# Optimization experiments

Measured on AMD Instinct MI355X. Metric: run time of the kernel, lower is better.

The kernel has to match this reference:

```python
import jax, jax.numpy as jnp
import numpy as np
import math

THETA = 10000.0

def apply_rope(x, start_pos=0):
    # x: [B, H, S, D], rotate-half RoPE
    B, H, S, D = x.shape
    pos = jnp.arange(start_pos, start_pos + S, dtype=jnp.float32)
    inv_freq = 1.0 / (THETA ** (jnp.arange(0, D, 2, dtype=jnp.float32) / D))  # [D/2]
    ang = pos[:, None] * inv_freq[None, :]  # [S, D/2]
    cos, sin = jnp.cos(ang), jnp.sin(ang)
    x1, x2 = jnp.split(x, 2, axis=-1)
    return jnp.concatenate([x1 * cos - x2 * sin, x1 * sin + x2 * cos], axis=-1)


def setup_inputs() -> dict:
    key = jax.random.key(0)
    ks = jax.random.split(key, 9)
    B, S, E, H, D = 2, 2048, 2048, 16, 128
    s = 0.02
    return {
        "x": jax.random.normal(ks[0], (B, S, E), jnp.float32),
        "W_q": jax.random.normal(ks[1], (E, H * D), jnp.float32) * s,
        "b_q": jnp.zeros((H * D,), jnp.float32),
        "W_k": jax.random.normal(ks[2], (E, D), jnp.float32) * s,
        "b_k": jnp.zeros((D,), jnp.float32),
        "W_v": jax.random.normal(ks[3], (E, D), jnp.float32) * s,
        "b_v": jnp.zeros((D,), jnp.float32),
        "W_o": jax.random.normal(ks[4], (H * D, E), jnp.float32) * s,
        "b_o": jnp.zeros((E,), jnp.float32),
    }


def reference(x, W_q, b_q, W_k, b_k, W_v, b_v, W_o, b_o):
    B, S, E = x.shape
    D = W_k.shape[1]
    H = W_q.shape[1] // D
    # projections (weights stored [in, out])
    q = (x @ W_q + b_q).reshape(B, S, H, D).transpose(0, 2, 1, 3)   # [B,H,S,D]
    k = (x @ W_k + b_k).reshape(B, S, 1, D).transpose(0, 2, 1, 3)   # [B,1,S,D]
    v = (x @ W_v + b_v).reshape(B, S, 1, D).transpose(0, 2, 1, 3)   # [B,1,S,D]
    # RoPE (cache is None -> start_pos = 0)
    q = apply_rope(q, 0)
    k = apply_rope(k, 0)
    # shared-KV attention: k head dim broadcasts over H q heads
    scores = jnp.einsum("bhqd,bokd->bhqk", q, k) / math.sqrt(D)     # [B,H,S,S]
    causal = jnp.tril(jnp.ones((S, S), dtype=bool))
    scores = jnp.where(causal, scores, -jnp.inf)
    attn = jax.nn.softmax(scores, axis=-1)
    out = jnp.einsum("bhqk,bokd->bhqd", attn, v)                    # [B,H,S,D]
    out = out.transpose(0, 2, 1, 3).reshape(B, S, H * D)
    out = out @ W_o + b_o                                           # dropout is identity in eval
    return out
```

## Files before the change

### kernel.cpp

```cpp
#include <hip/hip_runtime.h>
#include <stdint.h>

typedef __bf16 bf16x8 __attribute__((ext_vector_type(8)));
typedef __bf16 bf16x2 __attribute__((ext_vector_type(2)));
typedef float  f32x4  __attribute__((ext_vector_type(4)));
typedef short  s16x8  __attribute__((ext_vector_type(8)));

__device__ inline unsigned short f2b(float f) {
  unsigned int u = __builtin_bit_cast(unsigned int, f);
  u += 0x7FFFu + ((u >> 16) & 1u);
  return (unsigned short)(u >> 16);
}
__device__ inline float b2f(unsigned short h) {
  unsigned int u = ((unsigned int)h) << 16;
  return __builtin_bit_cast(float, u);
}
__device__ inline unsigned int pkcvt(float a, float b) {
  bf16x2 t;
  t[0] = (__bf16)a;
  t[1] = (__bf16)b;
  return __builtin_bit_cast(unsigned int, t);
}
__device__ inline void gload_lds16(const void* g, void* l) {
  __builtin_amdgcn_global_load_lds(
      (const __attribute__((address_space(1))) unsigned int*)g,
      (__attribute__((address_space(3))) unsigned int*)l, 16, 0, 0);
}

__global__ void k_cvt_bf16(const float* __restrict__ in, unsigned short* __restrict__ out, int n4) {
  int i = blockIdx.x * blockDim.x + threadIdx.x;
  if (i < n4) {
    float4 v = ((const float4*)in)[i];
    ushort4 o;
    o.x = f2b(v.x); o.y = f2b(v.y); o.z = f2b(v.z); o.w = f2b(v.w);
    ((ushort4*)out)[i] = o;
  }
}

__global__ void k_transpose(const float* __restrict__ Wq, const float* __restrict__ Wk,
                            const float* __restrict__ Wv, const float* __restrict__ Wo,
                            unsigned short* __restrict__ dstQKV, unsigned short* __restrict__ dstO) {
  __shared__ float tile[32][33];
  int n0 = blockIdx.x * 32;
  int k0 = blockIdx.y * 32;
  const float* src; int ldn, noff, K;
  unsigned short* dst;
  if (blockIdx.z == 0) {
    K = 2048; dst = dstQKV;
    if (n0 < 2048)       { src = Wq; ldn = 2048; noff = n0; }
    else if (n0 < 2176)  { src = Wk; ldn = 128;  noff = n0 - 2048; }
    else                 { src = Wv; ldn = 128;  noff = n0 - 2176; }
  } else {
    if (n0 >= 2048) return;
    K = 2048; dst = dstO;
    src = Wo; ldn = 2048; noff = n0;
  }
  int tx = threadIdx.x & 31, ty = threadIdx.x >> 5;
  for (int yy = ty; yy < 32; yy += 8)
    tile[yy][tx] = src[(size_t)(k0 + yy) * ldn + noff + tx];
  __syncthreads();
  for (int yy = ty; yy < 32; yy += 8)
    dst[(size_t)(n0 + yy) * K + k0 + tx] = f2b(tile[tx][yy]);
}

__global__ void k_bias_concat(const float* __restrict__ bq, const float* __restrict__ bk,
                              const float* __restrict__ bv, float* __restrict__ dst) {
  int i = blockIdx.x * 256 + threadIdx.x;
  if (i < 2304) dst[i] = (i < 2048) ? bq[i] : (i < 2176 ? bk[i - 2048] : bv[i - 2176]);
}

template<int OUT_BF16>
__global__ __launch_bounds__(256)
void k_gemm_lds(const unsigned short* __restrict__ A, const unsigned short* __restrict__ Bt,
                const float* __restrict__ bias, void* __restrict__ Cout,
                int M, int N, int K) {
  __shared__ unsigned short As[3][4096];
  __shared__ unsigned short Bs[3][4096];
  const int tid  = threadIdx.x;
  const int lane = tid & 63, wid = tid >> 6;
  const int lr = lane & 15, lk = lane >> 4;
  const int wr = wid >> 1,  wc = wid & 1;
  const int mb = blockIdx.y * 128, nb = blockIdx.x * 128;

  const int srow = tid >> 2, scb = (tid & 3) * 8;
  const size_t gA = (size_t)(mb + srow) * K + scb;
  const size_t gB = (size_t)(nb + srow) * K + scb;
  const int ldso = wid * 512;

  f32x4 acc[4][4];
  #pragma unroll
  for (int i = 0; i < 4; ++i)
    #pragma unroll
    for (int j = 0; j < 4; ++j) acc[i][j] = (f32x4){0.f, 0.f, 0.f, 0.f};

  auto stage = [&](int buf, int kt) {
    const size_t ko = (size_t)kt * 32;
    gload_lds16(A  + gA + ko,                  &As[buf][ldso]);
    gload_lds16(A  + gA + 64 * (size_t)K + ko, &As[buf][2048 + ldso]);
    gload_lds16(Bt + gB + ko,                  &Bs[buf][ldso]);
    gload_lds16(Bt + gB + 64 * (size_t)K + ko, &Bs[buf][2048 + ldso]);
  };

  const int ktn = K >> 5;
  stage(0, 0);
  stage(1, 1);

  int cur = 0;
  #pragma unroll 1
  for (int kt = 0; kt < ktn; ++kt) {
    if (kt + 2 < ktn) {
      int nbuf = cur + 2; if (nbuf >= 3) nbuf -= 3;
      stage(nbuf, kt + 2);
      asm volatile("s_waitcnt vmcnt(8)" ::: "memory");
    } else if (kt + 1 < ktn) {
      asm volatile("s_waitcnt vmcnt(4)" ::: "memory");
    } else {
      asm volatile("s_waitcnt vmcnt(0)" ::: "memory");
    }
    __builtin_amdgcn_sched_barrier(0);
    __builtin_amdgcn_s_barrier();
    bf16x8 af[4], bfv[4];
    #pragma unroll
    for (int m = 0; m < 4; ++m)
      af[m]  = *(const bf16x8*)&As[cur][(wr * 64 + m * 16 + lr) * 32 + lk * 8];
    #pragma unroll
    for (int n = 0; n < 4; ++n)
      bfv[n] = *(const bf16x8*)&Bs[cur][(wc * 64 + n * 16 + lr) * 32 + lk * 8];
    #pragma unroll
    for (int m = 0; m < 4; ++m)
      #pragma unroll
      for (int n = 0; n < 4; ++n)
        acc[m][n] = __builtin_amdgcn_mfma_f32_16x16x32_bf16(af[m], bfv[n], acc[m][n], 0, 0, 0);
    __builtin_amdgcn_s_barrier();
    ++cur; if (cur == 3) cur = 0;
  }

  const int r0 = mb + wr * 64, c0 = nb + wc * 64;
  #pragma unroll
  for (int m = 0; m < 4; ++m) {
    #pragma unroll
    for (int n = 0; n < 4; ++n) {
      int col = c0 + n * 16 + lr;
      float bb = bias[col];
      #pragma unroll
      for (int r = 0; r < 4; ++r) {
        int row = r0 + m * 16 + lk * 4 + r;
        float v = acc[m][n][r] + bb;
        if (OUT_BF16) ((unsigned short*)Cout)[(size_t)row * N + col] = f2b(v);
        else          ((float*)Cout)[(size_t)row * N + col] = v;
      }
    }
  }
}

__global__ void k_rope(const unsigned short* __restrict__ qkv,
                       unsigned short* __restrict__ qr,
                       unsigned short* __restrict__ kr,
                       int S, int H) {
  int R = blockIdx.x * 4 + (threadIdx.x >> 6);
  int lane = threadIdx.x & 63;
  int per_b = S * (H + 1);
  int b = R / per_b;
  int rem = R - b * per_b;
  int s = rem / (H + 1);
  int j = rem - s * (H + 1);
  const unsigned short* src = qkv + (size_t)(b * S + s) * 2304 + (j < H ? j * 128 : 2048);
  float x1 = b2f(src[lane]);
  float x2 = b2f(src[lane + 64]);
  float invf = expf(-(float)lane * (9.210340371976184f / 64.0f));
  float ang = (float)s * invf;
  float c = cosf(ang), sn = sinf(ang);
  float o1 = x1 * c - x2 * sn;
  float o2 = x1 * sn + x2 * c;
  unsigned short* dst;
  if (j < H) {
    const float scale = 0.08838834764831845f;
    o1 *= scale; o2 *= scale;
    dst = qr + ((size_t)(b * H + j) * S + s) * 128;
  } else {
    dst = kr + ((size_t)(b * S) + s) * 128;
  }
  dst[lane]      = f2b(o1);
  dst[lane + 64] = f2b(o2);
}

__global__ void k_vtrans(const unsigned short* __restrict__ qkv,
                         unsigned short* __restrict__ vt, int S) {
  __shared__ unsigned short tile[32][33];
  int b = blockIdx.z;
  int s0 = blockIdx.x * 32, d0 = blockIdx.y * 32;
  int tx = threadIdx.x & 31, ty = threadIdx.x >> 5;
  for (int yy = ty; yy < 32; yy += 8)
    tile[yy][tx] = qkv[(size_t)(b * S + s0 + yy) * 2304 + 2176 + d0 + tx];
  __syncthreads();
  for (int yy = ty; yy < 32; yy += 8)
    vt[((size_t)b * 128 + d0 + yy) * S + s0 + tx] = tile[tx][yy];
}

__global__ __launch_bounds__(256, 2)
void k_attn(const unsigned short* __restrict__ qr,
            const unsigned short* __restrict__ kr,
            const unsigned short* __restrict__ vt,
            unsigned short* __restrict__ attn_out,
            int S, int H) {
  const int b = blockIdx.z, h = blockIdx.y;
  const int qt = blockIdx.z ? (int)blockIdx.x : (gridDim.x - 1 - (int)blockIdx.x);
  const int qb0 = qt * 128;
  const int tid = threadIdx.x, wid = tid >> 6, lane = tid & 63;
  const int lr = lane & 15, lk = lane >> 4;
  const int qw = qb0 + wid * 32;

  __shared__ unsigned short Kt[2][64 * 128];
  __shared__ unsigned short Vt[2][128 * 64];

  const char* kbyte = (const char*)(kr + (size_t)b * S * 128);
  const char* vbyte = (const char*)(vt + (size_t)b * 128 * S);
  const size_t vrow_bytes = (size_t)S * 2;

  bf16x8 aq[2][4];
  #pragma unroll
  for (int g = 0; g < 2; ++g) {
    const unsigned short* qptr = qr + ((size_t)(b * H + h) * S + (qw + g * 16 + lr)) * 128;
    #pragma unroll
    for (int kk = 0; kk < 4; ++kk) aq[g][kk] = *(const bf16x8*)(qptr + kk * 32 + lk * 8);
  }

  f32x4 accO[2][8];
  #pragma unroll
  for (int g = 0; g < 2; ++g)
    #pragma unroll
    for (int t = 0; t < 8; ++t) accO[g][t] = (f32x4){0.f, 0.f, 0.f, 0.f};
  float lsum[2] = {0.f, 0.f};

  const int vsw = ((lr & 3) | ((lr >> 1) & 4)) << 4;
  int krow_[4], ksw_[4];
  #pragma unroll
  for (int m = 0; m < 4; ++m) {
    int row = ((m >> 1) << 5) + ((m & 1) << 2) + ((lr >> 2) << 3) + (lr & 3);
    krow_[m] = row;
    ksw_[m] = ((row & 3) | ((row >> 1) & 4)) << 4;
  }

  auto stage = [&](int buf, int kb) {
    const char* kg = kbyte + (size_t)kb * 256;
    #pragma unroll
    for (int r = 0; r < 4; ++r) {
      int row = (tid >> 4) + r * 16;
      int sw = ((row & 3) | ((row >> 1) & 4)) << 4;
      const char* src = kg + row * 256 + (((tid & 15) << 4) ^ sw);
      gload_lds16(src, (void*)((char*)&Kt[buf][0] + r * 4096 + wid * 1024));
    }
    const char* vg = vbyte + (size_t)kb * 2;
    #pragma unroll
    for (int r = 0; r < 4; ++r) {
      int d = (tid >> 3) + r * 32;
      int sw = ((d & 3) | ((d >> 1) & 4)) << 4;
      const char* src = vg + (size_t)d * vrow_bytes + (((tid & 7) << 4) ^ sw);
      gload_lds16(src, (void*)((char*)&Vt[buf][0] + r * 4096 + wid * 1024));
    }
  };

  const int nkv = (qb0 + 128) >> 6;
  stage(0, 0);
  int cur = 0;

  #pragma unroll 1
  for (int it = 0; it < nkv; ++it) {
    const int kb = it << 6;
    if (it + 1 < nkv) {
      stage(cur ^ 1, (it + 1) << 6);
      asm volatile("s_waitcnt vmcnt(8)" ::: "memory");
    } else {
      asm volatile("s_waitcnt vmcnt(0)" ::: "memory");
    }
    __builtin_amdgcn_sched_barrier(0);
    __builtin_amdgcn_s_barrier();

    if (kb <= qw + 31) {
      const unsigned short* Kc = &Kt[cur][0];
      const unsigned short* Vc = &Vt[cur][0];

      f32x4 s4[2][4];
      #pragma unroll
      for (int g = 0; g < 2; ++g)
        #pragma unroll
        for (int m = 0; m < 4; ++m) s4[g][m] = (f32x4){0.f, 0.f, 0.f, 0.f};
      __builtin_amdgcn_s_setprio(1);
      #pragma unroll
      for (int kk = 0; kk < 4; ++kk) {
        bf16x8 kfk[4];
        #pragma unroll
        for (int m = 0; m < 4; ++m)
          kfk[m] = *(const bf16x8*)((const char*)Kc + krow_[m] * 256 + ((kk * 64 + lk * 16) ^ ksw_[m]));
        #pragma unroll
        for (int m = 0; m < 4; ++m) {
          s4[0][m] = __builtin_amdgcn_mfma_f32_16x16x32_bf16(kfk[m], aq[0][kk], s4[0][m], 0, 0, 0);
          s4[1][m] = __builtin_amdgcn_mfma_f32_16x16x32_bf16(kfk[m], aq[1][kk], s4[1][m], 0, 0, 0);
        }
      }
      __builtin_amdgcn_s_setprio(0);

      bf16x8 pa[2][2];
      #pragma unroll
      for (int g = 0; g < 2; ++g) {
        const int rowq = qw + g * 16 + lr;
        const bool domask = (kb + 64) > (qw + g * 16);
        uint2 pk[4];
        #pragma unroll
        for (int m = 0; m < 4; ++m) {
          const int kb_m = kb + ((m >> 1) << 5) + ((m & 1) << 2) + lk * 8;
          float p[4];
          #pragma unroll
          for (int r = 0; r < 4; ++r) {
            float v = __expf(s4[g][m][r]);
            if (domask && (kb_m + r) > rowq) v = 0.f;
            p[r] = v;
            lsum[g] += v;
          }
          pk[m].x = pkcvt(p[0], p[1]);
          pk[m].y = pkcvt(p[2], p[3]);
        }
        uint4 ua, ub;
        ua.x = pk[0].x; ua.y = pk[0].y; ua.z = pk[1].x; ua.w = pk[1].y;
        ub.x = pk[2].x; ub.y = pk[2].y; ub.z = pk[3].x; ub.w = pk[3].y;
        pa[g][0] = __builtin_bit_cast(bf16x8, ua);
        pa[g][1] = __builtin_bit_cast(bf16x8, ub);
      }

      __builtin_amdgcn_s_setprio(1);
      #pragma unroll
      for (int t = 0; t < 8; ++t) {
        const char* vl = (const char*)(Vc + (t * 16 + lr) * 64);
        bf16x8 bv0 = *(const bf16x8*)(vl + ((lk * 16) ^ vsw));
        bf16x8 bv1 = *(const bf16x8*)(vl + ((64 + lk * 16) ^ vsw));
        accO[0][t] = __builtin_amdgcn_mfma_f32_16x16x32_bf16(pa[0][0], bv0, accO[0][t], 0, 0, 0);
        accO[1][t] = __builtin_amdgcn_mfma_f32_16x16x32_bf16(pa[1][0], bv0, accO[1][t], 0, 0, 0);
        accO[0][t] = __builtin_amdgcn_mfma_f32_16x16x32_bf16(pa[0][1], bv1, accO[0][t], 0, 0, 0);
        accO[1][t] = __builtin_amdgcn_mfma_f32_16x16x32_bf16(pa[1][1], bv1, accO[1][t], 0, 0, 0);
      }
      __builtin_amdgcn_s_setprio(0);
    }
    __builtin_amdgcn_s_barrier();
    cur ^= 1;
  }

  #pragma unroll
  for (int g = 0; g < 2; ++g) {
    float ls = lsum[g];
    ls += __shfl_xor(ls, 16);
    ls += __shfl_xor(ls, 32);
    float rl[4];
    #pragma unroll
    for (int r = 0; r < 4; ++r) rl[r] = 1.0f / __shfl(ls, lk * 4 + r);
    #pragma unroll
    for (int t = 0; t < 8; ++t) {
      #pragma unroll
      for (int r = 0; r < 4; ++r) {
        int srow = qw + g * 16 + lk * 4 + r;
        float o = accO[g][t][r] * rl[r];
        attn_out[((size_t)(b * S) + srow) * 2048 + h * 128 + t * 16 + lr] = f2b(o);
      }
    }
  }
}

extern "C" void kernel_launch(void* const* d_in, const int* in_sizes, int n_in,
                              void* d_out, int out_size, void* d_ws, size_t ws_size,
                              hipStream_t stream) {
  const float* x  = (const float*)d_in[0];
  const float* Wq = (const float*)d_in[1];
  const float* bq = (const float*)d_in[2];
  const float* Wk = (const float*)d_in[3];
  const float* bk = (const float*)d_in[4];
  const float* Wv = (const float*)d_in[5];
  const float* bv = (const float*)d_in[6];
  const float* Wo = (const float*)d_in[7];
  const float* bo = (const float*)d_in[8];

  const int B = 2, S = 2048, E = 2048, H = 16, D = 128;
  const int M = B * S;
  const int Nqkv = H * D + 2 * D;

  char* w = (char*)d_ws;
  unsigned short* xb    = (unsigned short*)w;
  unsigned short* WqkvT = (unsigned short*)(w + 16777216);
  unsigned short* qkv   = (unsigned short*)(w + 16777216 + 9437184);
  unsigned short* qr    = (unsigned short*)(w + 16777216 + 9437184 + 18874368);
  unsigned short* kr    = qr + (size_t)B * H * S * D;
  unsigned short* vtb   = kr + (size_t)B * S * D;
  float*          cbias = (float*)(vtb + (size_t)B * S * D);
  unsigned short* WoT   = (unsigned short*)(cbias + 4096);
  unsigned short* attn_out = xb;

  k_cvt_bf16<<<dim3((M * E / 4) / 256), 256, 0, stream>>>(x, xb, M * E / 4);
  k_transpose<<<dim3(Nqkv / 32, E / 32, 2), 256, 0, stream>>>(Wq, Wk, Wv, Wo, WqkvT, WoT);
  k_bias_concat<<<dim3(9), 256, 0, stream>>>(bq, bk, bv, cbias);
  k_gemm_lds<1><<<dim3(Nqkv / 128, M / 128), 256, 0, stream>>>(xb, WqkvT, cbias, (void*)qkv, M, Nqkv, E);
  k_rope<<<dim3(B * S * (H + 1) / 4), 256, 0, stream>>>(qkv, qr, kr, S, H);
  k_vtrans<<<dim3(S / 32, D / 32, B), 256, 0, stream>>>(qkv, vtb, S);
  k_attn<<<dim3(S / 128, H, B), 256, 0, stream>>>(qr, kr, vtb, attn_out, S, H);
  k_gemm_lds<0><<<dim3(E / 128, M / 128), 256, 0, stream>>>(attn_out, WoT, bo, (void*)d_out, M, E, H * D);
}
```

Baseline: 216.3 us.

## Pair causal query tiles per block with split-KV across two wave groups

The attention kernel now processes two query tiles per 512-thread block, a long tile (15-xp) and a short tile (xp), so every block does the same total causal work. Each 4-wave group walks a fixed 17-iteration KV schedule: group 0 handles the first half of tile A's KV range, and group 1 handles the rest of tile A and then all of tile B. The two partial results for tile A are combined through LDS at the end, which relies on the kernel having no running max (plain exp-sum). This is meant to remove the load imbalance from causal masking and the tail effect. In exchange it uses 128KB of LDS per block, doubles accumulator registers, and hardcodes S=2048 (the constants 15 and 17).

```diff
diff --git a/kernel.cpp b/kernel.cpp
--- a/kernel.cpp
+++ b/kernel.cpp
@@ -197,40 +197,56 @@
     vt[((size_t)b * 128 + d0 + yy) * S + s0 + tx] = tile[tx][yy];
 }
 
-__global__ __launch_bounds__(256, 2)
+__global__ __launch_bounds__(512, 2)
 void k_attn(const unsigned short* __restrict__ qr,
             const unsigned short* __restrict__ kr,
             const unsigned short* __restrict__ vt,
             unsigned short* __restrict__ attn_out,
             int S, int H) {
   const int b = blockIdx.z, h = blockIdx.y;
-  const int qt = blockIdx.z ? (int)blockIdx.x : (gridDim.x - 1 - (int)blockIdx.x);
-  const int qb0 = qt * 128;
+  const int xp = blockIdx.x;
+  const int qtA = 15 - xp;
+  const int qb0A = qtA * 128, qb0B = xp * 128;
+  const int nh = 2 * qtA + 2;
   const int tid = threadIdx.x, wid = tid >> 6, lane = tid & 63;
+  const int grp = wid >> 2, w4 = wid & 3;
   const int lr = lane & 15, lk = lane >> 4;
-  const int qw = qb0 + wid * 32;
-
-  __shared__ unsigned short Kt[2][64 * 128];
-  __shared__ unsigned short Vt[2][128 * 64];
+  const int gtid = tid & 255;
+
+  __shared__ __align__(16) char ldsbuf[131072];
+  char* gbase = ldsbuf + grp * 65536;
 
   const char* kbyte = (const char*)(kr + (size_t)b * S * 128);
   const char* vbyte = (const char*)(vt + (size_t)b * 128 * S);
   const size_t vrow_bytes = (size_t)S * 2;
 
-  bf16x8 aq[2][4];
-  #pragma unroll
-  for (int g = 0; g < 2; ++g) {
-    const unsigned short* qptr = qr + ((size_t)(b * H + h) * S + (qw + g * 16 + lr)) * 128;
-    #pragma unroll
-    for (int kk = 0; kk < 4; ++kk) aq[g][kk] = *(const bf16x8*)(qptr + kk * 32 + lk * 8);
-  }
-
-  f32x4 accO[2][8];
+  bf16x8 aqA[2][4], aqB[2][4];
+  {
+    const unsigned short* qa = qr + ((size_t)(b * H + h) * S + qb0A + w4 * 32) * 128;
+    #pragma unroll
+    for (int g = 0; g < 2; ++g)
+      #pragma unroll
+      for (int kk = 0; kk < 4; ++kk)
+        aqA[g][kk] = *(const bf16x8*)(qa + (size_t)(g * 16 + lr) * 128 + kk * 32 + lk * 8);
+    if (grp == 1) {
+      const unsigned short* qb = qr + ((size_t)(b * H + h) * S + qb0B + w4 * 32) * 128;
+      #pragma unroll
+      for (int g = 0; g < 2; ++g)
+        #pragma unroll
+        for (int kk = 0; kk < 4; ++kk)
+          aqB[g][kk] = *(const bf16x8*)(qb + (size_t)(g * 16 + lr) * 128 + kk * 32 + lk * 8);
+    }
+  }
+
+  f32x4 accA[2][8], accB[2][8];
   #pragma unroll
   for (int g = 0; g < 2; ++g)
     #pragma unroll
-    for (int t = 0; t < 8; ++t) accO[g][t] = (f32x4){0.f, 0.f, 0.f, 0.f};
-  float lsum[2] = {0.f, 0.f};
+    for (int t = 0; t < 8; ++t) {
+      accA[g][t] = (f32x4){0.f, 0.f, 0.f, 0.f};
+      accB[g][t] = (f32x4){0.f, 0.f, 0.f, 0.f};
+    }
+  float lsA[2] = {0.f, 0.f}, lsB[2] = {0.f, 0.f};
 
   const int vsw = ((lr & 3) | ((lr >> 1) & 4)) << 4;
   int krow_[4], ksw_[4];
@@ -245,120 +261,174 @@
     const char* kg = kbyte + (size_t)kb * 256;
     #pragma unroll
     for (int r = 0; r < 4; ++r) {
-      int row = (tid >> 4) + r * 16;
+      int row = (gtid >> 4) + r * 16;
       int sw = ((row & 3) | ((row >> 1) & 4)) << 4;
-      const char* src = kg + row * 256 + (((tid & 15) << 4) ^ sw);
-      gload_lds16(src, (void*)((char*)&Kt[buf][0] + r * 4096 + wid * 1024));
+      const char* src = kg + row * 256 + (((gtid & 15) << 4) ^ sw);
+      gload_lds16(src, (void*)(gbase + buf * 16384 + r * 4096 + w4 * 1024));
     }
     const char* vg = vbyte + (size_t)kb * 2;
     #pragma unroll
     for (int r = 0; r < 4; ++r) {
-      int d = (tid >> 3) + r * 32;
+      int d = (gtid >> 3) + r * 32;
       int sw = ((d & 3) | ((d >> 1) & 4)) << 4;
-      const char* src = vg + (size_t)d * vrow_bytes + (((tid & 7) << 4) ^ sw);
-      gload_lds16(src, (void*)((char*)&Vt[buf][0] + r * 4096 + wid * 1024));
+      const char* src = vg + (size_t)d * vrow_bytes + (((gtid & 7) << 4) ^ sw);
+      gload_lds16(src, (void*)(gbase + 32768 + buf * 16384 + r * 4096 + w4 * 1024));
     }
   };
 
-  const int nkv = (qb0 + 128) >> 6;
-  stage(0, 0);
+  auto itemKb = [&](int j, int& which) -> int {
+    if (grp == 0) { which = 0; return j * 64; }
+    int idx = 17 + j;
+    if (idx < nh) { which = 0; return idx * 64; }
+    which = 1; return (idx - nh) * 64;
+  };
+
+  auto computeTile = [&](const unsigned short* Kc, const unsigned short* Vc,
+                         int kb, int qb0cur, bf16x8 (&aq)[2][4],
+                         f32x4 (&acc)[2][8], float (&ls)[2]) {
+    const int qw = qb0cur + w4 * 32;
+    if (kb > qw + 31) return;
+    f32x4 s4[2][4];
+    #pragma unroll
+    for (int g = 0; g < 2; ++g)
+      #pragma unroll
+      for (int m = 0; m < 4; ++m) s4[g][m] = (f32x4){0.f, 0.f, 0.f, 0.f};
+    __builtin_amdgcn_s_setprio(1);
+    #pragma unroll
+    for (int kk = 0; kk < 4; ++kk) {
+      bf16x8 kfk[4];
+      #pragma unroll
+      for (int m = 0; m < 4; ++m)
+        kfk[m] = *(const bf16x8*)((const char*)Kc + krow_[m] * 256 + ((kk * 64 + lk * 16) ^ ksw_[m]));
+      #pragma unroll
+      for (int m = 0; m < 4; ++m) {
+        s4[0][m] = __builtin_amdgcn_mfma_f32_16x16x32_bf16(kfk[m], aq[0][kk], s4[0][m], 0, 0, 0);
+        s4[1][m] = __builtin_amdgcn_mfma_f32_16x16x32_bf16(kfk[m], aq[1][kk], s4[1][m], 0, 0, 0);
+      }
+    }
+    __builtin_amdgcn_s_setprio(0);
+    bf16x8 pa[2][2];
+    #pragma unroll
+    for (int g = 0; g < 2; ++g) {
+      const int rowq = qw + g * 16 + lr;
+      const bool domask = (kb + 64) > (qw + g * 16);
+      uint2 pk[4];
+      #pragma unroll
+      for (int m = 0; m < 4; ++m) {
+        const int kb_m = kb + ((m >> 1) << 5) + ((m & 1) << 2) + lk * 8;
+        float p[4];
+        #pragma unroll
+        for (int r = 0; r < 4; ++r) {
+          float v = __expf(s4[g][m][r]);
+          if (domask && (kb_m + r) > rowq) v = 0.f;
+          p[r] = v;
+          ls[g] += v;
+        }
+        pk[m].x = pkcvt(p[0], p[1]);
+        pk[m].y = pkcvt(p[2], p[3]);
+      }
+      uint4 ua, ub;
+      ua.x = pk[0].x; ua.y = pk[0].y; ua.z = pk[1].x; ua.w = pk[1].y;
+      ub.x = pk[2].x; ub.y = pk[2].y; ub.z = pk[3].x; ub.w = pk[3].y;
+      pa[g][0] = __builtin_bit_cast(bf16x8, ua);
+      pa[g][1] = __builtin_bit_cast(bf16x8, ub);
+    }
+    __builtin_amdgcn_s_setprio(1);
+    #pragma unroll
+    for (int t = 0; t < 8; ++t) {
+      const char* vl = (const char*)(Vc + (t * 16 + lr) * 64);
+      bf16x8 bv0 = *(const bf16x8*)(vl + ((lk * 16) ^ vsw));
+      bf16x8 bv1 = *(const bf16x8*)(vl + ((64 + lk * 16) ^ vsw));
+      acc[0][t] = __builtin_amdgcn_mfma_f32_16x16x32_bf16(pa[0][0], bv0, acc[0][t], 0, 0, 0);
+      acc[1][t] = __builtin_amdgcn_mfma_f32_16x16x32_bf16(pa[1][0], bv0, acc[1][t], 0, 0, 0);
+      acc[0][t] = __builtin_amdgcn_mfma_f32_16x16x32_bf16(pa[0][1], bv1, acc[0][t], 0, 0, 0);
+      acc[1][t] = __builtin_amdgcn_mfma_f32_16x16x32_bf16(pa[1][1], bv1, acc[1][t], 0, 0, 0);
+    }
+    __builtin_amdgcn_s_setprio(0);
+  };
+
+  {
+    int wh;
+    int kb0 = itemKb(0, wh);
+    stage(0, kb0);
+  }
   int cur = 0;
-
   #pragma unroll 1
-  for (int it = 0; it < nkv; ++it) {
-    const int kb = it << 6;
-    if (it + 1 < nkv) {
-      stage(cur ^ 1, (it + 1) << 6);
+  for (int j = 0; j < 17; ++j) {
+    if (j + 1 < 17) {
+      int wh;
+      stage(cur ^ 1, itemKb(j + 1, wh));
       asm volatile("s_waitcnt vmcnt(8)" ::: "memory");
     } else {
       asm volatile("s_waitcnt vmcnt(0)" ::: "memory");
     }
     __builtin_amdgcn_sched_barrier(0);
     __builtin_amdgcn_s_barrier();
-
-    if (kb <= qw + 31) {
-      const unsigned short* Kc = &Kt[cur][0];
-      const unsigned short* Vc = &Vt[cur][0];
-
-      f32x4 s4[2][4];
-      #pragma unroll
-      for (int g = 0; g < 2; ++g)
+    int wh;
+    const int kb = itemKb(j, wh);
+    const unsigned short* Kc = (const unsigned short*)(gbase + cur * 16384);
+    const unsigned short* Vc = (const unsigned short*)(gbase + 32768 + cur * 16384);
+    if (wh == 0) computeTile(Kc, Vc, kb, qb0A, aqA, accA, lsA);
+    else         computeTile(Kc, Vc, kb, qb0B, aqB, accB, lsB);
+    __builtin_amdgcn_s_barrier();
+    cur ^= 1;
+  }
+
+  float* comb  = (float*)ldsbuf;
+  float* lcomb = (float*)(ldsbuf + 128 * 132 * 4);
+  if (grp == 1) {
+    #pragma unroll
+    for (int g = 0; g < 2; ++g) {
+      #pragma unroll
+      for (int t = 0; t < 8; ++t)
         #pragma unroll
-        for (int m = 0; m < 4; ++m) s4[g][m] = (f32x4){0.f, 0.f, 0.f, 0.f};
-      __builtin_amdgcn_s_setprio(1);
-      #pragma unroll
-      for (int kk = 0; kk < 4; ++kk) {
-        bf16x8 kfk[4];
+        for (int r = 0; r < 4; ++r)
+          comb[(w4 * 32 + g * 16 + lk * 4 + r) * 132 + t * 16 + lr] = accA[g][t][r];
+      float v = lsA[g];
+      v += __shfl_xor(v, 16);
+      v += __shfl_xor(v, 32);
+      if (lk == 0) lcomb[w4 * 32 + g * 16 + lr] = v;
+    }
+  }
+  __syncthreads();
+  if (grp == 0) {
+    #pragma unroll
+    for (int g = 0; g < 2; ++g) {
+      float v = lsA[g];
+      v += __shfl_xor(v, 16);
+      v += __shfl_xor(v, 32);
+      v += lcomb[w4 * 32 + g * 16 + lr];
+      float rl[4];
+      #pragma unroll
+      for (int r = 0; r < 4; ++r) rl[r] = 1.0f / __shfl(v, lk * 4 + r);
+      #pragma unroll
+      for (int t = 0; t < 8; ++t) {
         #pragma unroll
-        for (int m = 0; m < 4; ++m)
-          kfk[m] = *(const bf16x8*)((const char*)Kc + krow_[m] * 256 + ((kk * 64 + lk * 16) ^ ksw_[m]));
-        #pragma unroll
-        for (int m = 0; m < 4; ++m) {
-          s4[0][m] = __builtin_amdgcn_mfma_f32_16x16x32_bf16(kfk[m], aq[0][kk], s4[0][m], 0, 0, 0);
-          s4[1][m] = __builtin_amdgcn_mfma_f32_16x16x32_bf16(kfk[m], aq[1][kk], s4[1][m], 0, 0, 0);
+        for (int r = 0; r < 4; ++r) {
+          int srow = qb0A + w4 * 32 + g * 16 + lk * 4 + r;
+          float o = (accA[g][t][r] +
+                     comb[(w4 * 32 + g * 16 + lk * 4 + r) * 132 + t * 16 + lr]) * rl[r];
+          attn_out[((size_t)(b * S) + srow) * 2048 + h * 128 + t * 16 + lr] = f2b(o);
         }
       }
-      __builtin_amdgcn_s_setprio(0);
-
-      bf16x8 pa[2][2];
-      #pragma unroll
-      for (int g = 0; g < 2; ++g) {
-        const int rowq = qw + g * 16 + lr;
-        const bool domask = (kb + 64) > (qw + g * 16);
-        uint2 pk[4];
+    }
+  } else {
+    #pragma unroll
+    for (int g = 0; g < 2; ++g) {
+      float v = lsB[g];
+      v += __shfl_xor(v, 16);
+      v += __shfl_xor(v, 32);
+      float rl[4];
+      #pragma unroll
+      for (int r = 0; r < 4; ++r) rl[r] = 1.0f / __shfl(v, lk * 4 + r);
+      #pragma unroll
+      for (int t = 0; t < 8; ++t) {
         #pragma unroll
-        for (int m = 0; m < 4; ++m) {
-          const int kb_m = kb + ((m >> 1) << 5) + ((m & 1) << 2) + lk * 8;
-          float p[4];
-          #pragma unroll
-          for (int r = 0; r < 4; ++r) {
-            float v = __expf(s4[g][m][r]);
-            if (domask && (kb_m + r) > rowq) v = 0.f;
-            p[r] = v;
-            lsum[g] += v;
-          }
-          pk[m].x = pkcvt(p[0], p[1]);
-          pk[m].y = pkcvt(p[2], p[3]);
+        for (int r = 0; r < 4; ++r) {
+          int srow = qb0B + w4 * 32 + g * 16 + lk * 4 + r;
+          float o = accB[g][t][r] * rl[r];
+          attn_out[((size_t)(b * S) + srow) * 2048 + h * 128 + t * 16 + lr] = f2b(o);
         }
-        uint4 ua, ub;
-        ua.x = pk[0].x; ua.y = pk[0].y; ua.z = pk[1].x; ua.w = pk[1].y;
-        ub.x = pk[2].x; ub.y = pk[2].y; ub.z = pk[3].x; ub.w = pk[3].y;
-        pa[g][0] = __builtin_bit_cast(bf16x8, ua);
-        pa[g][1] = __builtin_bit_cast(bf16x8, ub);
-      }
-
-      __builtin_amdgcn_s_setprio(1);
-      #pragma unroll
-      for (int t = 0; t < 8; ++t) {
-        const char* vl = (const char*)(Vc + (t * 16 + lr) * 64);
-        bf16x8 bv0 = *(const bf16x8*)(vl + ((lk * 16) ^ vsw));
-        bf16x8 bv1 = *(const bf16x8*)(vl + ((64 + lk * 16) ^ vsw));
-        accO[0][t] = __builtin_amdgcn_mfma_f32_16x16x32_bf16(pa[0][0], bv0, accO[0][t], 0, 0, 0);
-        accO[1][t] = __builtin_amdgcn_mfma_f32_16x16x32_bf16(pa[1][0], bv0, accO[1][t], 0, 0, 0);
-        accO[0][t] = __builtin_amdgcn_mfma_f32_16x16x32_bf16(pa[0][1], bv1, accO[0][t], 0, 0, 0);
-        accO[1][t] = __builtin_amdgcn_mfma_f32_16x16x32_bf16(pa[1][1], bv1, accO[1][t], 0, 0, 0);
-      }
-      __builtin_amdgcn_s_setprio(0);
-    }
-    __builtin_amdgcn_s_barrier();
-    cur ^= 1;
-  }
-
-  #pragma unroll
-  for (int g = 0; g < 2; ++g) {
-    float ls = lsum[g];
-    ls += __shfl_xor(ls, 16);
-    ls += __shfl_xor(ls, 32);
-    float rl[4];
-    #pragma unroll
-    for (int r = 0; r < 4; ++r) rl[r] = 1.0f / __shfl(ls, lk * 4 + r);
-    #pragma unroll
-    for (int t = 0; t < 8; ++t) {
-      #pragma unroll
-      for (int r = 0; r < 4; ++r) {
-        int srow = qw + g * 16 + lk * 4 + r;
-        float o = accO[g][t][r] * rl[r];
-        attn_out[((size_t)(b * S) + srow) * 2048 + h * 128 + t * 16 + lr] = f2b(o);
       }
     }
   }
@@ -398,6 +468,6 @@
   k_gemm_lds<1><<<dim3(Nqkv / 128, M / 128), 256, 0, stream>>>(xb, WqkvT, cbias, (void*)qkv, M, Nqkv, E);
   k_rope<<<dim3(B * S * (H + 1) / 4), 256, 0, stream>>>(qkv, qr, kr, S, H);
   k_vtrans<<<dim3(S / 32, D / 32, B), 256, 0, stream>>>(qkv, vtb, S);
-  k_attn<<<dim3(S / 128, H, B), 256, 0, stream>>>(qr, kr, vtb, attn_out, S, H);
+  k_attn<<<dim3(S / 256, H, B), 512, 0, stream>>>(qr, kr, vtb, attn_out, S, H);
   k_gemm_lds<0><<<dim3(E / 128, M / 128), 256, 0, stream>>>(attn_out, WoT, bo, (void*)d_out, M, E, H * D);
 }
```

Measured after the change: 236.9 us. +9.5%, slower.

## Balance causal attention by pairing query tiles and splitting work across two blocks

Applied to the files above, without the earlier changes.

The attention kernel now pairs a long query tile (8+p) with a short one (7-p), giving every pair 34 KV blocks that are split evenly into two blocks of 17 iterations each. The long tile's two partial results go to scratch buffers, and a new combine kernel sums and normalizes them. The change also folds the bias concat into the QKV GEMM epilogue and adds an XCD-aware block swizzle to the GEMM. The aim is to remove the load imbalance of causal tiles and a small launch, at the cost of extra scratch traffic and one more kernel.

```diff
diff --git a/kernel.cpp b/kernel.cpp
--- a/kernel.cpp
+++ b/kernel.cpp
@@ -63,16 +63,11 @@
     dst[(size_t)(n0 + yy) * K + k0 + tx] = f2b(tile[tx][yy]);
 }
 
-__global__ void k_bias_concat(const float* __restrict__ bq, const float* __restrict__ bk,
-                              const float* __restrict__ bv, float* __restrict__ dst) {
-  int i = blockIdx.x * 256 + threadIdx.x;
-  if (i < 2304) dst[i] = (i < 2048) ? bq[i] : (i < 2176 ? bk[i - 2048] : bv[i - 2176]);
-}
-
-template<int OUT_BF16>
+template<int OUT_BF16, int BIAS3>
 __global__ __launch_bounds__(256)
 void k_gemm_lds(const unsigned short* __restrict__ A, const unsigned short* __restrict__ Bt,
-                const float* __restrict__ bias, void* __restrict__ Cout,
+                const float* __restrict__ b0, const float* __restrict__ b1,
+                const float* __restrict__ b2, void* __restrict__ Cout,
                 int M, int N, int K) {
   __shared__ unsigned short As[3][4096];
   __shared__ unsigned short Bs[3][4096];
@@ -80,7 +75,12 @@
   const int lane = tid & 63, wid = tid >> 6;
   const int lr = lane & 15, lk = lane >> 4;
   const int wr = wid >> 1,  wc = wid & 1;
-  const int mb = blockIdx.y * 128, nb = blockIdx.x * 128;
+
+  const int nwg = gridDim.x * gridDim.y;
+  const int flat = blockIdx.y * gridDim.x + blockIdx.x;
+  const int swz = (flat & 7) * (nwg >> 3) + (flat >> 3);
+  const int mb = (swz / gridDim.x) * 128;
+  const int nb = (swz % gridDim.x) * 128;
 
   const int srow = tid >> 2, scb = (tid & 3) * 8;
   const size_t gA = (size_t)(mb + srow) * K + scb;
@@ -141,7 +141,9 @@
     #pragma unroll
     for (int n = 0; n < 4; ++n) {
       int col = c0 + n * 16 + lr;
-      float bb = bias[col];
+      float bb;
+      if (BIAS3) bb = (col < 2048) ? b0[col] : (col < 2176 ? b1[col - 2048] : b2[col - 2176]);
+      else       bb = b0[col];
       #pragma unroll
       for (int r = 0; r < 4; ++r) {
         int row = r0 + m * 16 + lk * 4 + r;
@@ -202,13 +204,21 @@
             const unsigned short* __restrict__ kr,
             const unsigned short* __restrict__ vt,
             unsigned short* __restrict__ attn_out,
+            unsigned short* __restrict__ pscr,
+            float* __restrict__ lscr,
             int S, int H) {
-  const int b = blockIdx.z, h = blockIdx.y;
-  const int qt = blockIdx.z ? (int)blockIdx.x : (gridDim.x - 1 - (int)blockIdx.x);
-  const int qb0 = qt * 128;
+  const int flat = blockIdx.x + 16 * blockIdx.y + 256 * blockIdx.z;
+  const int half = flat >> 8;
+  const int p    = flat & 7;
+  const int h    = (flat >> 3) & 15;
+  const int b    = (flat >> 7) & 1;
+  const int qtA = 8 + p, qtB = 7 - p;
+  const int qb0A = qtA * 128, qb0B = qtB * 128;
+  const int nA = 2 * qtA + 2;
+  const int pg = (b * H + h) * 8 + p;
+
   const int tid = threadIdx.x, wid = tid >> 6, lane = tid & 63;
   const int lr = lane & 15, lk = lane >> 4;
-  const int qw = qb0 + wid * 32;
 
   __shared__ unsigned short Kt[2][64 * 128];
   __shared__ unsigned short Vt[2][128 * 64];
@@ -218,19 +228,25 @@
   const size_t vrow_bytes = (size_t)S * 2;
 
   bf16x8 aq[2][4];
-  #pragma unroll
-  for (int g = 0; g < 2; ++g) {
-    const unsigned short* qptr = qr + ((size_t)(b * H + h) * S + (qw + g * 16 + lr)) * 128;
-    #pragma unroll
-    for (int kk = 0; kk < 4; ++kk) aq[g][kk] = *(const bf16x8*)(qptr + kk * 32 + lk * 8);
-  }
-
-  f32x4 accO[2][8];
-  #pragma unroll
-  for (int g = 0; g < 2; ++g)
-    #pragma unroll
-    for (int t = 0; t < 8; ++t) accO[g][t] = (f32x4){0.f, 0.f, 0.f, 0.f};
-  float lsum[2] = {0.f, 0.f};
+  auto loadQ = [&](int qb0) {
+    #pragma unroll
+    for (int g = 0; g < 2; ++g) {
+      const unsigned short* qptr = qr + ((size_t)(b * H + h) * S + (qb0 + wid * 32 + g * 16 + lr)) * 128;
+      #pragma unroll
+      for (int kk = 0; kk < 4; ++kk) aq[g][kk] = *(const bf16x8*)(qptr + kk * 32 + lk * 8);
+    }
+  };
+
+  f32x4 acc[2][8];
+  float ls[2];
+  auto resetAcc = [&]() {
+    #pragma unroll
+    for (int g = 0; g < 2; ++g) {
+      ls[g] = 0.f;
+      #pragma unroll
+      for (int t = 0; t < 8; ++t) acc[g][t] = (f32x4){0.f, 0.f, 0.f, 0.f};
+    }
+  };
 
   const int vsw = ((lr & 3) | ((lr >> 1) & 4)) << 4;
   int krow_[4], ksw_[4];
@@ -260,107 +276,183 @@
     }
   };
 
-  const int nkv = (qb0 + 128) >> 6;
-  stage(0, 0);
+  auto itemKb = [&](int j, int& which) -> int {
+    int idx = half * 17 + j;
+    if (idx < nA) { which = 0; return idx * 64; }
+    which = 1; return (idx - nA) * 64;
+  };
+
+  auto flushA = [&]() {
+    #pragma unroll
+    for (int g = 0; g < 2; ++g) {
+      float v = ls[g];
+      v += __shfl_xor(v, 16);
+      v += __shfl_xor(v, 32);
+      if (lk == 0) lscr[((size_t)pg * 2 + half) * 128 + wid * 32 + g * 16 + lr] = v;
+      #pragma unroll
+      for (int t = 0; t < 8; ++t)
+        #pragma unroll
+        for (int r = 0; r < 4; ++r) {
+          int row = wid * 32 + g * 16 + lk * 4 + r;
+          pscr[((size_t)pg * 2 + half) * 16384 + row * 128 + t * 16 + lr] = f2b(acc[g][t][r]);
+        }
+    }
+  };
+
+  auto computeTile = [&](int cur, int kb, int qb0cur) {
+    const int qw = qb0cur + wid * 32;
+    if (kb > qw + 31) return;
+    const unsigned short* Kc = &Kt[cur][0];
+    const unsigned short* Vc = &Vt[cur][0];
+    f32x4 s4[2][4];
+    #pragma unroll
+    for (int g = 0; g < 2; ++g)
+      #pragma unroll
+      for (int m = 0; m < 4; ++m) s4[g][m] = (f32x4){0.f, 0.f, 0.f, 0.f};
+    __builtin_amdgcn_s_setprio(1);
+    #pragma unroll
+    for (int kk = 0; kk < 4; ++kk) {
+      bf16x8 kfk[4];
+      #pragma unroll
+      for (int m = 0; m < 4; ++m)
+        kfk[m] = *(const bf16x8*)((const char*)Kc + krow_[m] * 256 + ((kk * 64 + lk * 16) ^ ksw_[m]));
+      #pragma unroll
+      for (int m = 0; m < 4; ++m) {
+        s4[0][m] = __builtin_amdgcn_mfma_f32_16x16x32_bf16(kfk[m], aq[0][kk], s4[0][m], 0, 0, 0);
+        s4[1][m] = __builtin_amdgcn_mfma_f32_16x16x32_bf16(kfk[m], aq[1][kk], s4[1][m], 0, 0, 0);
+      }
+    }
+    __builtin_amdgcn_s_setprio(0);
+    bf16x8 pa[2][2];
+    #pragma unroll
+    for (int g = 0; g < 2; ++g) {
+      const int rowq = qw + g * 16 + lr;
+      const bool domask = (kb + 64) > (qw + g * 16);
+      uint2 pk[4];
+      #pragma unroll
+      for (int m = 0; m < 4; ++m) {
+        const int kb_m = kb + ((m >> 1) << 5) + ((m & 1) << 2) + lk * 8;
+        float pv[4];
+        #pragma unroll
+        for (int r = 0; r < 4; ++r) {
+          float v = __expf(s4[g][m][r]);
+          if (domask && (kb_m + r) > rowq) v = 0.f;
+          pv[r] = v;
+          ls[g] += v;
+        }
+        pk[m].x = pkcvt(pv[0], pv[1]);
+        pk[m].y = pkcvt(pv[2], pv[3]);
+      }
+      uint4 ua, ub;
+      ua.x = pk[0].x; ua.y = pk[0].y; ua.z = pk[1].x; ua.w = pk[1].y;
+      ub.x = pk[2].x; ub.y = pk[2].y; ub.z = pk[3].x; ub.w = pk[3].y;
+      pa[g][0] = __builtin_bit_cast(bf16x8, ua);
+      pa[g][1] = __builtin_bit_cast(bf16x8, ub);
+    }
+    __builtin_amdgcn_s_setprio(1);
+    #pragma unroll
+    for (int t = 0; t < 8; ++t) {
+      const char* vl = (const char*)(Vc + (t * 16 + lr) * 64);
+      bf16x8 bv0 = *(const bf16x8*)(vl + ((lk * 16) ^ vsw));
+      bf16x8 bv1 = *(const bf16x8*)(vl + ((64 + lk * 16) ^ vsw));
+      acc[0][t] = __builtin_amdgcn_mfma_f32_16x16x32_bf16(pa[0][0], bv0, acc[0][t], 0, 0, 0);
+      acc[1][t] = __builtin_amdgcn_mfma_f32_16x16x32_bf16(pa[1][0], bv0, acc[1][t], 0, 0, 0);
+      acc[0][t] = __builtin_amdgcn_mfma_f32_16x16x32_bf16(pa[0][1], bv1, acc[0][t], 0, 0, 0);
+      acc[1][t] = __builtin_amdgcn_mfma_f32_16x16x32_bf16(pa[1][1], bv1, acc[1][t], 0, 0, 0);
+    }
+    __builtin_amdgcn_s_setprio(0);
+  };
+
+  loadQ(qb0A);
+  resetAcc();
+  int curTile = 0, qb0cur = qb0A;
+
+  {
+    int wh0;
+    stage(0, itemKb(0, wh0));
+  }
   int cur = 0;
-
   #pragma unroll 1
-  for (int it = 0; it < nkv; ++it) {
-    const int kb = it << 6;
-    if (it + 1 < nkv) {
-      stage(cur ^ 1, (it + 1) << 6);
+  for (int j = 0; j < 17; ++j) {
+    if (j + 1 < 17) {
+      int whn;
+      stage(cur ^ 1, itemKb(j + 1, whn));
       asm volatile("s_waitcnt vmcnt(8)" ::: "memory");
     } else {
       asm volatile("s_waitcnt vmcnt(0)" ::: "memory");
     }
     __builtin_amdgcn_sched_barrier(0);
     __builtin_amdgcn_s_barrier();
-
-    if (kb <= qw + 31) {
-      const unsigned short* Kc = &Kt[cur][0];
-      const unsigned short* Vc = &Vt[cur][0];
-
-      f32x4 s4[2][4];
-      #pragma unroll
-      for (int g = 0; g < 2; ++g)
+    int wh;
+    const int kb = itemKb(j, wh);
+    if (wh != curTile) {
+      flushA();
+      resetAcc();
+      loadQ(qb0B);
+      curTile = 1;
+      qb0cur = qb0B;
+    }
+    computeTile(cur, kb, qb0cur);
+    __builtin_amdgcn_s_barrier();
+    cur ^= 1;
+  }
+
+  if (half == 0) {
+    flushA();
+  } else {
+    #pragma unroll
+    for (int g = 0; g < 2; ++g) {
+      float v = ls[g];
+      v += __shfl_xor(v, 16);
+      v += __shfl_xor(v, 32);
+      float rl[4];
+      #pragma unroll
+      for (int r = 0; r < 4; ++r) rl[r] = 1.0f / __shfl(v, lk * 4 + r);
+      #pragma unroll
+      for (int t = 0; t < 8; ++t) {
         #pragma unroll
-        for (int m = 0; m < 4; ++m) s4[g][m] = (f32x4){0.f, 0.f, 0.f, 0.f};
-      __builtin_amdgcn_s_setprio(1);
-      #pragma unroll
-      for (int kk = 0; kk < 4; ++kk) {
-        bf16x8 kfk[4];
-        #pragma unroll
-        for (int m = 0; m < 4; ++m)
-          kfk[m] = *(const bf16x8*)((const char*)Kc + krow_[m] * 256 + ((kk * 64 + lk * 16) ^ ksw_[m]));
-        #pragma unroll
-        for (int m = 0; m < 4; ++m) {
-          s4[0][m] = __builtin_amdgcn_mfma_f32_16x16x32_bf16(kfk[m], aq[0][kk], s4[0][m], 0, 0, 0);
-          s4[1][m] = __builtin_amdgcn_mfma_f32_16x16x32_bf16(kfk[m], aq[1][kk], s4[1][m], 0, 0, 0);
+        for (int r = 0; r < 4; ++r) {
+          int srow = qb0B + wid * 32 + g * 16 + lk * 4 + r;
+          float o = acc[g][t][r] * rl[r];
+          attn_out[((size_t)(b * S) + srow) * 2048 + h * 128 + t * 16 + lr] = f2b(o);
         }
       }
-      __builtin_amdgcn_s_setprio(0);
-
-      bf16x8 pa[2][2];
-      #pragma unroll
-      for (int g = 0; g < 2; ++g) {
-        const int rowq = qw + g * 16 + lr;
-        const bool domask = (kb + 64) > (qw + g * 16);
-        uint2 pk[4];
-        #pragma unroll
-        for (int m = 0; m < 4; ++m) {
-          const int kb_m = kb + ((m >> 1) << 5) + ((m & 1) << 2) + lk * 8;
-          float p[4];
-          #pragma unroll
-          for (int r = 0; r < 4; ++r) {
-            float v = __expf(s4[g][m][r]);
-            if (domask && (kb_m + r) > rowq) v = 0.f;
-            p[r] = v;
-            lsum[g] += v;
-          }
-          pk[m].x = pkcvt(p[0], p[1]);
-          pk[m].y = pkcvt(p[2], p[3]);
-        }
-        uint4 ua, ub;
-        ua.x = pk[0].x; ua.y = pk[0].y; ua.z = pk[1].x; ua.w = pk[1].y;
-        ub.x = pk[2].x; ub.y = pk[2].y; ub.z = pk[3].x; ub.w = pk[3].y;
-        pa[g][0] = __builtin_bit_cast(bf16x8, ua);
-        pa[g][1] = __builtin_bit_cast(bf16x8, ub);
-      }
-
-      __builtin_amdgcn_s_setprio(1);
-      #pragma unroll
-      for (int t = 0; t < 8; ++t) {
-        const char* vl = (const char*)(Vc + (t * 16 + lr) * 64);
-        bf16x8 bv0 = *(const bf16x8*)(vl + ((lk * 16) ^ vsw));
-        bf16x8 bv1 = *(const bf16x8*)(vl + ((64 + lk * 16) ^ vsw));
-        accO[0][t] = __builtin_amdgcn_mfma_f32_16x16x32_bf16(pa[0][0], bv0, accO[0][t], 0, 0, 0);
-        accO[1][t] = __builtin_amdgcn_mfma_f32_16x16x32_bf16(pa[1][0], bv0, accO[1][t], 0, 0, 0);
-        accO[0][t] = __builtin_amdgcn_mfma_f32_16x16x32_bf16(pa[0][1], bv1, accO[0][t], 0, 0, 0);
-        accO[1][t] = __builtin_amdgcn_mfma_f32_16x16x32_bf16(pa[1][1], bv1, accO[1][t], 0, 0, 0);
-      }
-      __builtin_amdgcn_s_setprio(0);
-    }
-    __builtin_amdgcn_s_barrier();
-    cur ^= 1;
-  }
-
+    }
+  }
+}
+
+__global__ void k_combine(const unsigned short* __restrict__ pscr,
+                          const float* __restrict__ lscr,
+                          unsigned short* __restrict__ attn_out, int S, int H) {
+  const int p = blockIdx.x, h = blockIdx.y, b = blockIdx.z;
+  const int pg = (b * H + h) * 8 + p;
+  const int qb0A = (8 + p) * 128;
+  const int tid = threadIdx.x;
+  const unsigned short* p0 = pscr + (size_t)pg * 2 * 16384;
+  const unsigned short* p1 = p0 + 16384;
+  const float* l0 = lscr + (size_t)pg * 2 * 128;
+  const float* l1 = l0 + 128;
   #pragma unroll
-  for (int g = 0; g < 2; ++g) {
-    float ls = lsum[g];
-    ls += __shfl_xor(ls, 16);
-    ls += __shfl_xor(ls, 32);
-    float rl[4];
-    #pragma unroll
-    for (int r = 0; r < 4; ++r) rl[r] = 1.0f / __shfl(ls, lk * 4 + r);
-    #pragma unroll
-    for (int t = 0; t < 8; ++t) {
-      #pragma unroll
-      for (int r = 0; r < 4; ++r) {
-        int srow = qw + g * 16 + lk * 4 + r;
-        float o = accO[g][t][r] * rl[r];
-        attn_out[((size_t)(b * S) + srow) * 2048 + h * 128 + t * 16 + lr] = f2b(o);
-      }
-    }
+  for (int it = 0; it < 8; ++it) {
+    int row = it * 16 + (tid >> 4);
+    int col = (tid & 15) * 8;
+    float rl = 1.0f / (l0[row] + l1[row]);
+    ushort4 a = *(const ushort4*)(p0 + row * 128 + col);
+    ushort4 c = *(const ushort4*)(p1 + row * 128 + col);
+    ushort4 a2 = *(const ushort4*)(p0 + row * 128 + col + 4);
+    ushort4 c2 = *(const ushort4*)(p1 + row * 128 + col + 4);
+    ushort4 o1, o2;
+    o1.x = f2b((b2f(a.x) + b2f(c.x)) * rl);
+    o1.y = f2b((b2f(a.y) + b2f(c.y)) * rl);
+    o1.z = f2b((b2f(a.z) + b2f(c.z)) * rl);
+    o1.w = f2b((b2f(a.w) + b2f(c.w)) * rl);
+    o2.x = f2b((b2f(a2.x) + b2f(c2.x)) * rl);
+    o2.y = f2b((b2f(a2.y) + b2f(c2.y)) * rl);
+    o2.z = f2b((b2f(a2.z) + b2f(c2.z)) * rl);
+    o2.w = f2b((b2f(a2.w) + b2f(c2.w)) * rl);
+    unsigned short* dst = attn_out + ((size_t)(b * S) + qb0A + row) * 2048 + h * 128 + col;
+    *(ushort4*)dst = o1;
+    *(ushort4*)(dst + 4) = o2;
   }
 }
 
@@ -391,13 +483,15 @@
   float*          cbias = (float*)(vtb + (size_t)B * S * D);
   unsigned short* WoT   = (unsigned short*)(cbias + 4096);
   unsigned short* attn_out = xb;
+  unsigned short* pscr  = qkv;
+  float*          lscr  = (float*)WqkvT;
 
   k_cvt_bf16<<<dim3((M * E / 4) / 256), 256, 0, stream>>>(x, xb, M * E / 4);
   k_transpose<<<dim3(Nqkv / 32, E / 32, 2), 256, 0, stream>>>(Wq, Wk, Wv, Wo, WqkvT, WoT);
-  k_bias_concat<<<dim3(9), 256, 0, stream>>>(bq, bk, bv, cbias);
-  k_gemm_lds<1><<<dim3(Nqkv / 128, M / 128), 256, 0, stream>>>(xb, WqkvT, cbias, (void*)qkv, M, Nqkv, E);
+  k_gemm_lds<1, 1><<<dim3(Nqkv / 128, M / 128), 256, 0, stream>>>(xb, WqkvT, bq, bk, bv, (void*)qkv, M, Nqkv, E);
   k_rope<<<dim3(B * S * (H + 1) / 4), 256, 0, stream>>>(qkv, qr, kr, S, H);
   k_vtrans<<<dim3(S / 32, D / 32, B), 256, 0, stream>>>(qkv, vtb, S);
-  k_attn<<<dim3(S / 128, H, B), 256, 0, stream>>>(qr, kr, vtb, attn_out, S, H);
-  k_gemm_lds<0><<<dim3(E / 128, M / 128), 256, 0, stream>>>(attn_out, WoT, bo, (void*)d_out, M, E, H * D);
-}
+  k_attn<<<dim3(16, 16, 2), 256, 0, stream>>>(qr, kr, vtb, attn_out, pscr, lscr, S, H);
+  k_combine<<<dim3(8, H, B), 256, 0, stream>>>(pscr, lscr, attn_out, S, H);
+  k_gemm_lds<0, 0><<<dim3(E / 128, M / 128), 256, 0, stream>>>(attn_out, WoT, bo, nullptr, nullptr, (void*)d_out, M, E, H * D);
+}
```

Result: faster. 196.4 us (-9.2%).
